# Performance work log

Measured on AMD Instinct MI355X. Metric: run time of the kernel, lower is better.

Reference implementation:

```python
import jax, jax.numpy as jnp
import numpy as np
import math

N_HEAD, D_MODEL, D_K, D_V = 8, 512, 64, 64
B, S = 4, 2048
EPS = 1e-5

def _xavier(key, shape):
    fan_in, fan_out = shape
    a = math.sqrt(6.0 / (fan_in + fan_out))
    return jax.random.uniform(key, shape, jnp.float32, -a, a)

def setup_inputs() -> dict:
    key = jax.random.key(0)
    ks = jax.random.split(key, 8)
    q = jax.random.normal(ks[0], (B, S, D_MODEL), jnp.float32)
    k = jax.random.normal(ks[1], (B, S, D_MODEL), jnp.float32)
    v = jax.random.normal(ks[2], (B, S, D_MODEL), jnp.float32)
    mask = jax.random.uniform(ks[3], (B, S, S)) < 0.1
    w_q = _xavier(ks[4], (D_MODEL, N_HEAD * D_K))
    w_k = _xavier(ks[5], (D_MODEL, N_HEAD * D_K))
    w_v = _xavier(ks[6], (D_MODEL, N_HEAD * D_V))
    w_o = _xavier(ks[7], (D_MODEL, N_HEAD * D_V))
    ln_g = jnp.ones((D_MODEL,), jnp.float32)
    ln_b = jnp.zeros((D_MODEL,), jnp.float32)
    return {"q": q, "k": k, "v": v, "w_q": w_q, "w_k": w_k, "w_v": w_v,
            "w_o": w_o, "ln_g": ln_g, "ln_b": ln_b, "mask": mask}

def reference(q, k, v, w_q, w_k, w_v, w_o, ln_g, ln_b, mask):
    b, lq, _ = q.shape
    lk = k.shape[1]
    residual = q
    # projections + head split: [b, len, H, d] -> [b, H, len, d]
    qh = (q @ w_q).reshape(b, lq, N_HEAD, D_K).transpose(0, 2, 1, 3)
    kh = (k @ w_k).reshape(b, lk, N_HEAD, D_K).transpose(0, 2, 1, 3)
    vh = (v @ w_v).reshape(b, lk, N_HEAD, D_V).transpose(0, 2, 1, 3)
    scale = math.sqrt(D_K)
    attn = jnp.einsum('bhqd,bhkd->bhqk', qh, kh) / scale
    attn = jnp.where(mask[:, None, :, :], jnp.float32(-1e9), attn)
    attn = jax.nn.softmax(attn, axis=-1)  # dropout is identity in eval
    heads = jnp.einsum('bhqk,bhkd->bhqd', attn, vh)
    heads = heads.transpose(0, 2, 1, 3).reshape(b, lq, N_HEAD * D_V)
    out = heads @ w_o + residual
    mu = out.mean(-1, keepdims=True)
    var = ((out - mu) ** 2).mean(-1, keepdims=True)
    out = (out - mu) * jax.lax.rsqrt(var + EPS) * ln_g + ln_b
    return out, attn
```

## Files before the change

kernel.cpp:

```cpp
#include <hip/hip_runtime.h>
#include <cstddef>

typedef __attribute__((ext_vector_type(8))) short bf16x8;
typedef __attribute__((ext_vector_type(4))) float f32x4;
typedef __attribute__((ext_vector_type(2))) float f32x2;
typedef __attribute__((ext_vector_type(4))) short short4v;
typedef unsigned long long u64;
typedef unsigned int u32;
typedef unsigned short u16;

#define MFMA16 __builtin_amdgcn_mfma_f32_16x16x32_bf16
static constexpr float LN_EPS = 1e-5f;
static constexpr float L2E = 1.44269504f;

__device__ __forceinline__ u16 f2bf(float f) {
    u32 u = __builtin_bit_cast(u32, f);
    return (u16)((u + 0x7FFFu + ((u >> 16) & 1u)) >> 16);
}
__device__ __forceinline__ float bf2f(u16 h) {
    u32 u = ((u32)h) << 16;
    return __builtin_bit_cast(float, u);
}

__device__ __forceinline__ float block_sum256(float v) {
    __shared__ float sc[4];
    #pragma unroll
    for (int o = 32; o > 0; o >>= 1) v += __shfl_down(v, o);
    if ((threadIdx.x & 63) == 0) sc[threadIdx.x >> 6] = v;
    __syncthreads();
    v = sc[0] + sc[1] + sc[2] + sc[3];
    __syncthreads();
    return v;
}

__global__ __launch_bounds__(256) void prepw_kernel(
    const float* __restrict__ wq, const float* __restrict__ wk,
    const float* __restrict__ wv, const float* __restrict__ wo,
    u16* __restrict__ wt)
{
    const int mat = blockIdx.z;
    const float* W = mat == 0 ? wq : mat == 1 ? wk : mat == 2 ? wv : wo;
    const int k0 = blockIdx.x * 64, n0 = blockIdx.y * 64;
    __shared__ u16 ld[64][72];
    const int t = threadIdx.x;
    {
        const int kk = t >> 2;
        #pragma unroll
        for (int j = 0; j < 4; ++j) {
            const int nn = ((t & 3) + j * 4) * 4;
            float4 x = *(const float4*)&W[(size_t)(k0 + kk) * 512 + n0 + nn];
            ld[kk][nn + 0] = f2bf(x.x); ld[kk][nn + 1] = f2bf(x.y);
            ld[kk][nn + 2] = f2bf(x.z); ld[kk][nn + 3] = f2bf(x.w);
        }
    }
    __syncthreads();
    {
        const int n = t & 63, kc = (t >> 6) * 16;
        u16* op = wt + ((size_t)mat * 512 + n0 + n) * 512 + k0 + kc;
        #pragma unroll
        for (int j = 0; j < 4; ++j) {
            short4v v;
            v[0] = ld[kc + j*4 + 0][n]; v[1] = ld[kc + j*4 + 1][n];
            v[2] = ld[kc + j*4 + 2][n]; v[3] = ld[kc + j*4 + 3][n];
            *(short4v*)(op + j * 4) = v;
        }
    }
}

__global__ __launch_bounds__(256) void prepm_kernel(
    const int* __restrict__ mask, u64* __restrict__ bits)
{
    const int t = threadIdx.x;
    const int row = blockIdx.x * 4 + (t >> 6);
    const int wl = t & 63;
    const int* mrow = mask + (size_t)row * 2048;
    u64* brow = bits + (size_t)row * 32;
    #pragma unroll 8
    for (int it = 0; it < 32; ++it) {
        u64 b = __ballot(mrow[it * 64 + wl] != 0);
        if (wl == 0) brow[it] = b;
    }
}

__global__ __launch_bounds__(256) void proj_kernel(
    const float* __restrict__ qin, const float* __restrict__ kin, const float* __restrict__ vin,
    const u16* __restrict__ wt,
    u16* __restrict__ Qh, u16* __restrict__ Kh, u16* __restrict__ Vt)
{
    const int z = blockIdx.z;
    const float* X = z == 0 ? qin : (z == 1 ? kin : vin);
    const u16* W = wt + (size_t)z * 512 * 512;
    const int m0 = blockIdx.x * 64;
    const int h = blockIdx.y;
    const int t = threadIdx.x, l = t & 63, w = t >> 6;
    const int q = l & 15, G = l >> 4;
    const int wr = w >> 1, wc = w & 1;

    f32x4 acc[2][2] = {};
    for (int k0 = 0; k0 < 512; k0 += 32) {
        bf16x8 af[2], bfr[2];
        #pragma unroll
        for (int mi = 0; mi < 2; ++mi) {
            const float* xp = X + (size_t)(m0 + wr*32 + mi*16 + q) * 512 + k0 + G*8;
            float4 x0 = *(const float4*)xp;
            float4 x1 = *(const float4*)(xp + 4);
            bf16x8 a;
            a[0] = f2bf(x0.x); a[1] = f2bf(x0.y); a[2] = f2bf(x0.z); a[3] = f2bf(x0.w);
            a[4] = f2bf(x1.x); a[5] = f2bf(x1.y); a[6] = f2bf(x1.z); a[7] = f2bf(x1.w);
            af[mi] = a;
        }
        #pragma unroll
        for (int tn = 0; tn < 2; ++tn)
            bfr[tn] = *(const bf16x8*)(W + (size_t)(h*64 + wc*32 + tn*16 + q) * 512 + k0 + G*8);
        #pragma unroll
        for (int mi = 0; mi < 2; ++mi)
            #pragma unroll
            for (int tn = 0; tn < 2; ++tn)
                acc[mi][tn] = MFMA16(af[mi], bfr[tn], acc[mi][tn], 0, 0, 0);
    }
    if (z == 2) {
        #pragma unroll
        for (int mi = 0; mi < 2; ++mi)
            #pragma unroll
            for (int tn = 0; tn < 2; ++tn) {
                const int d = wc*32 + tn*16 + q;
                const int m = m0 + wr*32 + mi*16 + G*4;
                const int bb = m >> 11, s = m & 2047;
                short4v sv;
                #pragma unroll
                for (int r = 0; r < 4; ++r) sv[r] = (short)f2bf(acc[mi][tn][r]);
                *(short4v*)&Vt[(((size_t)(bb*8 + h) << 6) + d) * 2048 + s] = sv;
            }
    } else {
        u16* O = z == 0 ? Qh : Kh;
        const float scv = (z == 0) ? 0.125f : 1.0f;
        #pragma unroll
        for (int mi = 0; mi < 2; ++mi)
            #pragma unroll
            for (int tn = 0; tn < 2; ++tn)
                #pragma unroll
                for (int r = 0; r < 4; ++r) {
                    const int m = m0 + wr*32 + mi*16 + G*4 + r;
                    const int bb = m >> 11, s = m & 2047;
                    const int d = wc*32 + tn*16 + q;
                    O[(((size_t)(bb*8 + h) << 11) + s) * 64 + d] = f2bf(acc[mi][tn][r] * scv);
                }
    }
}

__global__ __launch_bounds__(256, 4) void attnpv_kernel(
    const u16* __restrict__ Qh, const u16* __restrict__ Kh, const u16* __restrict__ Vt,
    const u64* __restrict__ bits,
    float* __restrict__ attn, u16* __restrict__ heads)
{
    const int j   = blockIdx.x;
    const int lid = (j & 7) * 128 + (j >> 3);
    const int qt = lid & 31, bh = lid >> 5;
    const int b = bh >> 3, h = bh & 7;
    const int m0 = qt * 64;
    const int t = threadIdx.x, l = t & 63, w = t >> 6;
    const int q = l & 15, G = l >> 4;
    const int qrow = m0 + w*16 + q;
    __shared__ u16 kbuf[2][4096];
    __shared__ u16 vbuf[2][4096];
    __shared__ u16 alds[4][1024];
    u16* my = alds[w];

    const size_t qbase = (((size_t)bh << 11) + qrow) * 64;
    bf16x8 qf0 = *(const bf16x8*)(Qh + qbase + G*8);
    bf16x8 qf1 = *(const bf16x8*)(Qh + qbase + 32 + G*8);
    const u64* brow = bits + (((size_t)b << 11) + qrow) * 32;
    const int swz = (q & 7) << 3;

    const int srow0 = t >> 3;
    const int scol  = (t & 7) * 8;
    const u16* Kbase = Kh + (((size_t)bh << 11) * 64);
    const u16* Vbase = Vt + (((size_t)bh << 6) * 2048);
    const int eswz = (t * 8) ^ ((srow0 & 7) << 3);

    bf16x8 sk0, sk1, sv0, sv1;
    float rs = 0.f;

    {
        const u16* kp = Kbase + (size_t)srow0 * 64 + scol;
        sk0 = *(const bf16x8*)kp;
        sk1 = *(const bf16x8*)(kp + 32 * 64);
        *(bf16x8*)&kbuf[0][eswz]        = sk0;
        *(bf16x8*)&kbuf[0][2048 + eswz] = sk1;
    }
    __syncthreads();
    for (int kt = 0; kt < 32; ++kt) {
        const int cur = kt & 1;
        if (kt < 31) {
            const u16* kp = Kbase + (size_t)((kt + 1) * 64 + srow0) * 64 + scol;
            sk0 = *(const bf16x8*)kp;
            sk1 = *(const bf16x8*)(kp + 32 * 64);
        }
        f32x4 acc[4] = {};
        #pragma unroll
        for (int mt = 0; mt < 4; ++mt) {
            const int r = mt*16 + q;
            const int rsw = (r & 7) << 3;
            bf16x8 k0 = *(const bf16x8*)&kbuf[cur][(r*64 +      G*8) ^ rsw];
            bf16x8 k1 = *(const bf16x8*)&kbuf[cur][(r*64 + 32 + G*8) ^ rsw];
            acc[mt] = MFMA16(k0, qf0, acc[mt], 0, 0, 0);
            acc[mt] = MFMA16(k1, qf1, acc[mt], 0, 0, 0);
        }
        const u64 mw = brow[kt];
        #pragma unroll
        for (int mt = 0; mt < 4; ++mt)
            #pragma unroll
            for (int r = 0; r < 4; ++r) {
                const int c = mt*16 + G*4 + r;
                rs += ((mw >> c) & 1) ? 0.f : exp2f(acc[mt][r] * L2E);
            }
        if (kt < 31) {
            *(bf16x8*)&kbuf[cur ^ 1][eswz]        = sk0;
            *(bf16x8*)&kbuf[cur ^ 1][2048 + eswz] = sk1;
        }
        __syncthreads();
    }
    rs += __shfl_xor(rs, 16);
    rs += __shfl_xor(rs, 32);
    const float inv = 1.0f / rs;

    f32x4 pacc[4] = {};
    {
        const u16* kp = Kbase + (size_t)srow0 * 64 + scol;
        sk0 = *(const bf16x8*)kp;
        sk1 = *(const bf16x8*)(kp + 32 * 64);
        const u16* vp = Vbase + (size_t)srow0 * 2048 + scol;
        sv0 = *(const bf16x8*)vp;
        sv1 = *(const bf16x8*)(vp + 32 * 2048);
        *(bf16x8*)&kbuf[0][eswz]        = sk0;
        *(bf16x8*)&kbuf[0][2048 + eswz] = sk1;
        *(bf16x8*)&vbuf[0][eswz]        = sv0;
        *(bf16x8*)&vbuf[0][2048 + eswz] = sv1;
    }
    __syncthreads();
    for (int kt = 0; kt < 32; ++kt) {
        const int cur = kt & 1;
        if (kt < 31) {
            const int n1 = (kt + 1) * 64;
            const u16* kp = Kbase + (size_t)(n1 + srow0) * 64 + scol;
            sk0 = *(const bf16x8*)kp;
            sk1 = *(const bf16x8*)(kp + 32 * 64);
            const u16* vp = Vbase + (size_t)srow0 * 2048 + n1 + scol;
            sv0 = *(const bf16x8*)vp;
            sv1 = *(const bf16x8*)(vp + 32 * 2048);
        }
        f32x4 acc[4] = {};
        #pragma unroll
        for (int mt = 0; mt < 4; ++mt) {
            const int r = mt*16 + q;
            const int rsw = (r & 7) << 3;
            bf16x8 k0 = *(const bf16x8*)&kbuf[cur][(r*64 +      G*8) ^ rsw];
            bf16x8 k1 = *(const bf16x8*)&kbuf[cur][(r*64 + 32 + G*8) ^ rsw];
            acc[mt] = MFMA16(k0, qf0, acc[mt], 0, 0, 0);
            acc[mt] = MFMA16(k1, qf1, acc[mt], 0, 0, 0);
        }
        const u64 mw = brow[kt];
        #pragma unroll
        for (int mt = 0; mt < 4; ++mt) {
            short4v sv;
            #pragma unroll
            for (int r = 0; r < 4; ++r) {
                const int c = mt*16 + G*4 + r;
                const float e = ((mw >> c) & 1) ? 0.f : exp2f(acc[mt][r] * L2E);
                sv[r] = (short)f2bf(e);
            }
            *(short4v*)&my[(q*64 + mt*16 + G*4) ^ swz] = sv;
        }
        bf16x8 an0 = *(const bf16x8*)&my[(q*64 +  0 + G*8) ^ swz];
        bf16x8 an1 = *(const bf16x8*)&my[(q*64 + 32 + G*8) ^ swz];
        #pragma unroll
        for (int dmt = 0; dmt < 4; ++dmt) {
            const int r = dmt*16 + q;
            const int rsw = (r & 7) << 3;
            bf16x8 v0 = *(const bf16x8*)&vbuf[cur][(r*64 +      G*8) ^ rsw];
            bf16x8 v1 = *(const bf16x8*)&vbuf[cur][(r*64 + 32 + G*8) ^ rsw];
            pacc[dmt] = MFMA16(v0, an0, pacc[dmt], 0, 0, 0);
            pacc[dmt] = MFMA16(v1, an1, pacc[dmt], 0, 0, 0);
        }
        if (kt < 31) {
            const int nxt = cur ^ 1;
            *(bf16x8*)&kbuf[nxt][eswz]        = sk0;
            *(bf16x8*)&kbuf[nxt][2048 + eswz] = sk1;
            *(bf16x8*)&vbuf[nxt][eswz]        = sv0;
            *(bf16x8*)&vbuf[nxt][2048 + eswz] = sv1;
        }
        {
            const int rr = (l >> 5) * 8;
            float* awbase = attn + ((((size_t)bh << 11) + m0 + w*16) << 11) + kt*64 + (l & 31)*2;
            #pragma unroll
            for (int it = 0; it < 8; ++it) {
                const int r = rr + it;
                const float iv = __shfl(inv, r);
                const u32 e2 = *(const u32*)&my[(r*64 + (l & 31)*2) ^ ((r & 7) << 3)];
                f32x2 o;
                o[0] = bf2f((u16)(e2 & 0xffffu)) * iv;
                o[1] = bf2f((u16)(e2 >> 16))     * iv;
                *(f32x2*)(awbase + (size_t)r * 2048) = o;
            }
        }
        __syncthreads();
    }
    #pragma unroll
    for (int dmt = 0; dmt < 4; ++dmt) {
        short4v sv;
        #pragma unroll
        for (int r = 0; r < 4; ++r) sv[r] = (short)f2bf(pacc[dmt][r] * inv);
        *(short4v*)&heads[(((size_t)b << 11) + qrow) * 512 + h*64 + dmt*16 + G*4] = sv;
    }
}

__global__ __launch_bounds__(256) void outgemm_kernel(
    const u16* __restrict__ heads, const u16* __restrict__ wt,
    const float* __restrict__ qin, float* __restrict__ out)
{
    const int m0 = blockIdx.x * 64, n0b = blockIdx.y * 64;
    const int t = threadIdx.x, l = t & 63, w = t >> 6;
    const int q = l & 15, G = l >> 4;
    const int wr = w >> 1, wc = w & 1;
    const u16* W = wt + (size_t)3 * 512 * 512;
    f32x4 acc[2][2] = {};
    for (int k0 = 0; k0 < 512; k0 += 32) {
        bf16x8 af[2], bfr[2];
        #pragma unroll
        for (int mi = 0; mi < 2; ++mi)
            af[mi] = *(const bf16x8*)(heads + (size_t)(m0 + wr*32 + mi*16 + q) * 512 + k0 + G*8);
        #pragma unroll
        for (int tn = 0; tn < 2; ++tn)
            bfr[tn] = *(const bf16x8*)(W + (size_t)(n0b + wc*32 + tn*16 + q) * 512 + k0 + G*8);
        #pragma unroll
        for (int mi = 0; mi < 2; ++mi)
            #pragma unroll
            for (int tn = 0; tn < 2; ++tn)
                acc[mi][tn] = MFMA16(af[mi], bfr[tn], acc[mi][tn], 0, 0, 0);
    }
    #pragma unroll
    for (int mi = 0; mi < 2; ++mi)
        #pragma unroll
        for (int r = 0; r < 4; ++r) {
            const int m = m0 + wr*32 + mi*16 + G*4 + r;
            #pragma unroll
            for (int tn = 0; tn < 2; ++tn) {
                const int n = n0b + wc*32 + tn*16 + q;
                out[(size_t)m * 512 + n] = acc[mi][tn][r] + qin[(size_t)m * 512 + n];
            }
        }
}

__global__ __launch_bounds__(256) void ln_kernel(
    float* __restrict__ out, const float* __restrict__ g, const float* __restrict__ be)
{
    const int m = blockIdx.x;
    float* row = out + (size_t)m * 512;
    const int t = threadIdx.x;
    float2 v = ((const float2*)row)[t];
    float s  = block_sum256(v.x + v.y);
    float s2 = block_sum256(v.x * v.x + v.y * v.y);
    const float mu  = s * (1.0f / 512.0f);
    const float var = s2 * (1.0f / 512.0f) - mu * mu;
    const float inv = rsqrtf(var + LN_EPS);
    float2 gg = ((const float2*)g)[t];
    float2 bb = ((const float2*)be)[t];
    float2 r;
    r.x = (v.x - mu) * inv * gg.x + bb.x;
    r.y = (v.y - mu) * inv * gg.y + bb.y;
    ((float2*)row)[t] = r;
}

extern "C" void kernel_launch(void* const* d_in, const int* in_sizes, int n_in,
                              void* d_out, int out_size, void* d_ws, size_t ws_size,
                              hipStream_t stream) {
    const float* q   = (const float*)d_in[0];
    const float* k   = (const float*)d_in[1];
    const float* v   = (const float*)d_in[2];
    const float* wq  = (const float*)d_in[3];
    const float* wk  = (const float*)d_in[4];
    const float* wv  = (const float*)d_in[5];
    const float* wo  = (const float*)d_in[6];
    const float* g   = (const float*)d_in[7];
    const float* be  = (const float*)d_in[8];
    const int*   msk = (const int*)d_in[9];

    float* out  = (float*)d_out;
    float* attn = out + (size_t)4 * 2048 * 512;

    const size_t nQKV = (size_t)32 * 2048 * 64;
    u16* Qh    = (u16*)d_ws;
    u16* Kh    = Qh + nQKV;
    u16* Vt    = Kh + nQKV;
    u16* heads = Vt + nQKV;
    u16* wt    = heads + (size_t)8192 * 512;
    u64* bits  = (u64*)(wt + (size_t)4 * 512 * 512);

    prepw_kernel  <<<dim3(8, 8, 4),    256, 0, stream>>>(wq, wk, wv, wo, wt);
    prepm_kernel  <<<dim3(2048),       256, 0, stream>>>(msk, bits);
    proj_kernel   <<<dim3(128, 8, 3),  256, 0, stream>>>(q, k, v, wt, Qh, Kh, Vt);
    attnpv_kernel <<<dim3(1024),       256, 0, stream>>>(Qh, Kh, Vt, bits, attn, heads);
    outgemm_kernel<<<dim3(128, 8),     256, 0, stream>>>(heads, wt, q, out);
    ln_kernel     <<<dim3(8192),       256, 0, stream>>>(out, g, be);
}
```

Before: 469.6 us.

## Process two query tiles per attention block to reuse K/V shared tiles

Each attention block now handles two 64-row query tiles (qt and qt+16) instead of one, so every K and V tile loaded into shared memory feeds twice as many MFMAs and the grid shrinks from 1024 to 512 blocks. The softmax normalisers move into shared memory for the attention-matrix writeback, and that writeback is interleaved across rows. This halves K/V global traffic and the number of barrier rounds per query row. The cost is more registers and LDS per block, the loss of the 4-blocks-per-CU launch bound, and fewer blocks to spread over the CUs. The kernel is likely dominated by the large fp32 attention-matrix write, which this change does not reduce.

```diff
diff --git a/kernel.cpp b/kernel.cpp
--- a/kernel.cpp
+++ b/kernel.cpp
@@ -148,28 +148,34 @@
     }
 }
 
-__global__ __launch_bounds__(256, 4) void attnpv_kernel(
+__global__ __launch_bounds__(256) void attnpv_kernel(
     const u16* __restrict__ Qh, const u16* __restrict__ Kh, const u16* __restrict__ Vt,
     const u64* __restrict__ bits,
     float* __restrict__ attn, u16* __restrict__ heads)
 {
     const int j   = blockIdx.x;
-    const int lid = (j & 7) * 128 + (j >> 3);
-    const int qt = lid & 31, bh = lid >> 5;
+    const int lid = (j & 7) * 64 + (j >> 3);
+    const int qt = lid & 15, bh = lid >> 4;
     const int b = bh >> 3, h = bh & 7;
-    const int m0 = qt * 64;
+    const int m0A = qt * 64, m0B = (qt + 16) * 64;
     const int t = threadIdx.x, l = t & 63, w = t >> 6;
     const int q = l & 15, G = l >> 4;
-    const int qrow = m0 + w*16 + q;
+    const int qrowA = m0A + w*16 + q, qrowB = m0B + w*16 + q;
     __shared__ u16 kbuf[2][4096];
     __shared__ u16 vbuf[2][4096];
-    __shared__ u16 alds[4][1024];
-    u16* my = alds[w];
-
-    const size_t qbase = (((size_t)bh << 11) + qrow) * 64;
-    bf16x8 qf0 = *(const bf16x8*)(Qh + qbase + G*8);
-    bf16x8 qf1 = *(const bf16x8*)(Qh + qbase + 32 + G*8);
-    const u64* brow = bits + (((size_t)b << 11) + qrow) * 32;
+    __shared__ u16 alds[4][2048];
+    __shared__ float sinv[2][64];
+    u16* myA = alds[w];
+    u16* myB = alds[w] + 1024;
+
+    const size_t qbaseA = (((size_t)bh << 11) + qrowA) * 64;
+    const size_t qbaseB = (((size_t)bh << 11) + qrowB) * 64;
+    bf16x8 qfA0 = *(const bf16x8*)(Qh + qbaseA + G*8);
+    bf16x8 qfA1 = *(const bf16x8*)(Qh + qbaseA + 32 + G*8);
+    bf16x8 qfB0 = *(const bf16x8*)(Qh + qbaseB + G*8);
+    bf16x8 qfB1 = *(const bf16x8*)(Qh + qbaseB + 32 + G*8);
+    const u64* browA = bits + (((size_t)b << 11) + qrowA) * 32;
+    const u64* browB = bits + (((size_t)b << 11) + qrowB) * 32;
     const int swz = (q & 7) << 3;
 
     const int srow0 = t >> 3;
@@ -179,7 +185,7 @@
     const int eswz = (t * 8) ^ ((srow0 & 7) << 3);
 
     bf16x8 sk0, sk1, sv0, sv1;
-    float rs = 0.f;
+    float rsA = 0.f, rsB = 0.f;
 
     {
         const u16* kp = Kbase + (size_t)srow0 * 64 + scol;
@@ -196,23 +202,27 @@
             sk0 = *(const bf16x8*)kp;
             sk1 = *(const bf16x8*)(kp + 32 * 64);
         }
-        f32x4 acc[4] = {};
+        f32x4 accA[4] = {}, accB[4] = {};
         #pragma unroll
         for (int mt = 0; mt < 4; ++mt) {
             const int r = mt*16 + q;
             const int rsw = (r & 7) << 3;
             bf16x8 k0 = *(const bf16x8*)&kbuf[cur][(r*64 +      G*8) ^ rsw];
             bf16x8 k1 = *(const bf16x8*)&kbuf[cur][(r*64 + 32 + G*8) ^ rsw];
-            acc[mt] = MFMA16(k0, qf0, acc[mt], 0, 0, 0);
-            acc[mt] = MFMA16(k1, qf1, acc[mt], 0, 0, 0);
-        }
-        const u64 mw = brow[kt];
+            accA[mt] = MFMA16(k0, qfA0, accA[mt], 0, 0, 0);
+            accA[mt] = MFMA16(k1, qfA1, accA[mt], 0, 0, 0);
+            accB[mt] = MFMA16(k0, qfB0, accB[mt], 0, 0, 0);
+            accB[mt] = MFMA16(k1, qfB1, accB[mt], 0, 0, 0);
+        }
+        const u64 mwA = browA[kt];
+        const u64 mwB = browB[kt];
         #pragma unroll
         for (int mt = 0; mt < 4; ++mt)
             #pragma unroll
             for (int r = 0; r < 4; ++r) {
                 const int c = mt*16 + G*4 + r;
-                rs += ((mw >> c) & 1) ? 0.f : exp2f(acc[mt][r] * L2E);
+                rsA += ((mwA >> c) & 1) ? 0.f : exp2f(accA[mt][r] * L2E);
+                rsB += ((mwB >> c) & 1) ? 0.f : exp2f(accB[mt][r] * L2E);
             }
         if (kt < 31) {
             *(bf16x8*)&kbuf[cur ^ 1][eswz]        = sk0;
@@ -220,11 +230,15 @@
         }
         __syncthreads();
     }
-    rs += __shfl_xor(rs, 16);
-    rs += __shfl_xor(rs, 32);
-    const float inv = 1.0f / rs;
-
-    f32x4 pacc[4] = {};
+    rsA += __shfl_xor(rsA, 16);
+    rsA += __shfl_xor(rsA, 32);
+    rsB += __shfl_xor(rsB, 16);
+    rsB += __shfl_xor(rsB, 32);
+    const float invA = 1.0f / rsA;
+    const float invB = 1.0f / rsB;
+    if (G == 0) { sinv[0][w*16 + q] = invA; sinv[1][w*16 + q] = invB; }
+
+    f32x4 paccA[4] = {}, paccB[4] = {};
     {
         const u16* kp = Kbase + (size_t)srow0 * 64 + scol;
         sk0 = *(const bf16x8*)kp;
@@ -249,38 +263,68 @@
             sv0 = *(const bf16x8*)vp;
             sv1 = *(const bf16x8*)(vp + 32 * 2048);
         }
-        f32x4 acc[4] = {};
-        #pragma unroll
-        for (int mt = 0; mt < 4; ++mt) {
-            const int r = mt*16 + q;
-            const int rsw = (r & 7) << 3;
-            bf16x8 k0 = *(const bf16x8*)&kbuf[cur][(r*64 +      G*8) ^ rsw];
-            bf16x8 k1 = *(const bf16x8*)&kbuf[cur][(r*64 + 32 + G*8) ^ rsw];
-            acc[mt] = MFMA16(k0, qf0, acc[mt], 0, 0, 0);
-            acc[mt] = MFMA16(k1, qf1, acc[mt], 0, 0, 0);
-        }
-        const u64 mw = brow[kt];
-        #pragma unroll
-        for (int mt = 0; mt < 4; ++mt) {
-            short4v sv;
-            #pragma unroll
-            for (int r = 0; r < 4; ++r) {
-                const int c = mt*16 + G*4 + r;
-                const float e = ((mw >> c) & 1) ? 0.f : exp2f(acc[mt][r] * L2E);
-                sv[r] = (short)f2bf(e);
-            }
-            *(short4v*)&my[(q*64 + mt*16 + G*4) ^ swz] = sv;
-        }
-        bf16x8 an0 = *(const bf16x8*)&my[(q*64 +  0 + G*8) ^ swz];
-        bf16x8 an1 = *(const bf16x8*)&my[(q*64 + 32 + G*8) ^ swz];
+        {
+            f32x4 acc[4] = {};
+            #pragma unroll
+            for (int mt = 0; mt < 4; ++mt) {
+                const int r = mt*16 + q;
+                const int rsw = (r & 7) << 3;
+                bf16x8 k0 = *(const bf16x8*)&kbuf[cur][(r*64 +      G*8) ^ rsw];
+                bf16x8 k1 = *(const bf16x8*)&kbuf[cur][(r*64 + 32 + G*8) ^ rsw];
+                acc[mt] = MFMA16(k0, qfA0, acc[mt], 0, 0, 0);
+                acc[mt] = MFMA16(k1, qfA1, acc[mt], 0, 0, 0);
+            }
+            const u64 mw = browA[kt];
+            #pragma unroll
+            for (int mt = 0; mt < 4; ++mt) {
+                short4v sv;
+                #pragma unroll
+                for (int r = 0; r < 4; ++r) {
+                    const int c = mt*16 + G*4 + r;
+                    const float e = ((mw >> c) & 1) ? 0.f : exp2f(acc[mt][r] * L2E);
+                    sv[r] = (short)f2bf(e);
+                }
+                *(short4v*)&myA[(q*64 + mt*16 + G*4) ^ swz] = sv;
+            }
+        }
+        {
+            f32x4 acc[4] = {};
+            #pragma unroll
+            for (int mt = 0; mt < 4; ++mt) {
+                const int r = mt*16 + q;
+                const int rsw = (r & 7) << 3;
+                bf16x8 k0 = *(const bf16x8*)&kbuf[cur][(r*64 +      G*8) ^ rsw];
+                bf16x8 k1 = *(const bf16x8*)&kbuf[cur][(r*64 + 32 + G*8) ^ rsw];
+                acc[mt] = MFMA16(k0, qfB0, acc[mt], 0, 0, 0);
+                acc[mt] = MFMA16(k1, qfB1, acc[mt], 0, 0, 0);
+            }
+            const u64 mw = browB[kt];
+            #pragma unroll
+            for (int mt = 0; mt < 4; ++mt) {
+                short4v sv;
+                #pragma unroll
+                for (int r = 0; r < 4; ++r) {
+                    const int c = mt*16 + G*4 + r;
+                    const float e = ((mw >> c) & 1) ? 0.f : exp2f(acc[mt][r] * L2E);
+                    sv[r] = (short)f2bf(e);
+                }
+                *(short4v*)&myB[(q*64 + mt*16 + G*4) ^ swz] = sv;
+            }
+        }
+        bf16x8 anA0 = *(const bf16x8*)&myA[(q*64 +  0 + G*8) ^ swz];
+        bf16x8 anA1 = *(const bf16x8*)&myA[(q*64 + 32 + G*8) ^ swz];
+        bf16x8 anB0 = *(const bf16x8*)&myB[(q*64 +  0 + G*8) ^ swz];
+        bf16x8 anB1 = *(const bf16x8*)&myB[(q*64 + 32 + G*8) ^ swz];
         #pragma unroll
         for (int dmt = 0; dmt < 4; ++dmt) {
             const int r = dmt*16 + q;
             const int rsw = (r & 7) << 3;
             bf16x8 v0 = *(const bf16x8*)&vbuf[cur][(r*64 +      G*8) ^ rsw];
             bf16x8 v1 = *(const bf16x8*)&vbuf[cur][(r*64 + 32 + G*8) ^ rsw];
-            pacc[dmt] = MFMA16(v0, an0, pacc[dmt], 0, 0, 0);
-            pacc[dmt] = MFMA16(v1, an1, pacc[dmt], 0, 0, 0);
+            paccA[dmt] = MFMA16(v0, anA0, paccA[dmt], 0, 0, 0);
+            paccA[dmt] = MFMA16(v1, anA1, paccA[dmt], 0, 0, 0);
+            paccB[dmt] = MFMA16(v0, anB0, paccB[dmt], 0, 0, 0);
+            paccB[dmt] = MFMA16(v1, anB1, paccB[dmt], 0, 0, 0);
         }
         if (kt < 31) {
             const int nxt = cur ^ 1;
@@ -290,27 +334,39 @@
             *(bf16x8*)&vbuf[nxt][2048 + eswz] = sv1;
         }
         {
-            const int rr = (l >> 5) * 8;
-            float* awbase = attn + ((((size_t)bh << 11) + m0 + w*16) << 11) + kt*64 + (l & 31)*2;
+            const int rr = l >> 5;
+            const int cc = (l & 31) * 2;
+            float* awA = attn + ((((size_t)bh << 11) + m0A + w*16) << 11) + kt*64 + cc;
+            float* awB = attn + ((((size_t)bh << 11) + m0B + w*16) << 11) + kt*64 + cc;
             #pragma unroll
             for (int it = 0; it < 8; ++it) {
-                const int r = rr + it;
-                const float iv = __shfl(inv, r);
-                const u32 e2 = *(const u32*)&my[(r*64 + (l & 31)*2) ^ ((r & 7) << 3)];
-                f32x2 o;
-                o[0] = bf2f((u16)(e2 & 0xffffu)) * iv;
-                o[1] = bf2f((u16)(e2 >> 16))     * iv;
-                *(f32x2*)(awbase + (size_t)r * 2048) = o;
+                const int r = it*2 + rr;
+                const int off = (r*64 + cc) ^ ((r & 7) << 3);
+                const u32 eA = *(const u32*)&myA[off];
+                const u32 eB = *(const u32*)&myB[off];
+                const float ivA = sinv[0][w*16 + r];
+                const float ivB = sinv[1][w*16 + r];
+                f32x2 oA, oB;
+                oA[0] = bf2f((u16)(eA & 0xffffu)) * ivA;
+                oA[1] = bf2f((u16)(eA >> 16))     * ivA;
+                oB[0] = bf2f((u16)(eB & 0xffffu)) * ivB;
+                oB[1] = bf2f((u16)(eB >> 16))     * ivB;
+                *(f32x2*)(awA + (size_t)r * 2048) = oA;
+                *(f32x2*)(awB + (size_t)r * 2048) = oB;
             }
         }
         __syncthreads();
     }
     #pragma unroll
     for (int dmt = 0; dmt < 4; ++dmt) {
-        short4v sv;
-        #pragma unroll
-        for (int r = 0; r < 4; ++r) sv[r] = (short)f2bf(pacc[dmt][r] * inv);
-        *(short4v*)&heads[(((size_t)b << 11) + qrow) * 512 + h*64 + dmt*16 + G*4] = sv;
+        short4v svA, svB;
+        #pragma unroll
+        for (int r = 0; r < 4; ++r) {
+            svA[r] = (short)f2bf(paccA[dmt][r] * invA);
+            svB[r] = (short)f2bf(paccB[dmt][r] * invB);
+        }
+        *(short4v*)&heads[(((size_t)b << 11) + qrowA) * 512 + h*64 + dmt*16 + G*4] = svA;
+        *(short4v*)&heads[(((size_t)b << 11) + qrowB) * 512 + h*64 + dmt*16 + G*4] = svB;
     }
 }
 
@@ -399,7 +455,7 @@
     prepw_kernel  <<<dim3(8, 8, 4),    256, 0, stream>>>(wq, wk, wv, wo, wt);
     prepm_kernel  <<<dim3(2048),       256, 0, stream>>>(msk, bits);
     proj_kernel   <<<dim3(128, 8, 3),  256, 0, stream>>>(q, k, v, wt, Qh, Kh, Vt);
-    attnpv_kernel <<<dim3(1024),       256, 0, stream>>>(Qh, Kh, Vt, bits, attn, heads);
+    attnpv_kernel <<<dim3(512),        256, 0, stream>>>(Qh, Kh, Vt, bits, attn, heads);
     outgemm_kernel<<<dim3(128, 8),     256, 0, stream>>>(heads, wt, q, out);
     ln_kernel     <<<dim3(8192),       256, 0, stream>>>(out, g, be);
 }
```

Result: faster. 447.5 us (-4.7%).
